# Optimization experiments

Measured on AMD Instinct MI355X. Metric: run time of the kernel, lower is better.

The kernel has to match this reference:

```python
import jax, jax.numpy as jnp
import numpy as np

N = 50000        # nodes
E = 800000       # edges
F_IN = 64
HID = [128, 256, 256]
G = 512          # graphs in batch
C = 6            # classes
EPS = 1e-5


def setup_inputs() -> dict:
    key = jax.random.key(0)
    ks = jax.random.split(key, 32)
    inp = {}
    inp['x'] = jax.random.normal(ks[0], (N, F_IN), dtype=jnp.float32)
    inp['edge_index'] = jax.random.randint(ks[1], (2, E), 0, N, dtype=jnp.int64)
    inp['batch'] = jnp.sort(jax.random.randint(ks[2], (N,), 0, G, dtype=jnp.int64))
    dims = [F_IN] + HID
    i = 3
    for l in range(3):
        d_in, d_out = dims[l], dims[l + 1]
        inp[f'W{l+1}'] = jax.random.normal(ks[i], (d_in, d_out), dtype=jnp.float32) * (1.0 / np.sqrt(d_in)); i += 1
        inp[f'b{l+1}'] = jnp.zeros((d_out,), dtype=jnp.float32)
        inp[f'g{l+1}'] = jnp.ones((d_out,), dtype=jnp.float32)
        inp[f'be{l+1}'] = jnp.zeros((d_out,), dtype=jnp.float32)
        inp[f'm{l+1}'] = jax.random.normal(ks[i], (d_out,), dtype=jnp.float32) * 0.1; i += 1
        inp[f'v{l+1}'] = jax.random.uniform(ks[i], (d_out,), dtype=jnp.float32, minval=0.5, maxval=1.5); i += 1
    mlp_dims = [(2 * HID[-1], 256), (256, 128), (128, C)]
    for l, (d_in, d_out) in enumerate(mlp_dims):
        inp[f'Wm{l+1}'] = jax.random.normal(ks[i], (d_in, d_out), dtype=jnp.float32) * (1.0 / np.sqrt(d_in)); i += 1
        inp[f'bm{l+1}'] = jnp.zeros((d_out,), dtype=jnp.float32)
    return inp


def _forward(x, edge_index, batch,
             W1, b1, g1, be1, m1, v1,
             W2, b2, g2, be2, m2, v2,
             W3, b3, g3, be3, m3, v3,
             Wm1, bm1, Wm2, bm2, Wm3, bm3):
    src, dst = edge_index[0], edge_index[1]
    loops = jnp.arange(N, dtype=src.dtype)
    src_sl = jnp.concatenate([src, loops])   # self-loops, as in PyG GCNConv
    dst_sl = jnp.concatenate([dst, loops])
    deg = jax.ops.segment_sum(jnp.ones_like(src_sl, dtype=x.dtype), dst_sl, num_segments=N)
    dis = jnp.where(deg > 0, jax.lax.rsqrt(deg), 0.0)
    norm = dis[src_sl] * dis[dst_sl]          # [E+N]

    def gcn(h, W, b):
        h = h @ W                              # transform first (PyG order)
        msg = h[src_sl] * norm[:, None]        # gather + scale
        return jax.ops.segment_sum(msg, dst_sl, num_segments=N) + b

    def bn_relu(h, g, be, m, v):
        return jax.nn.relu((h - m) * jax.lax.rsqrt(v + EPS) * g + be)

    h = bn_relu(gcn(x, W1, b1), g1, be1, m1, v1)
    h = bn_relu(gcn(h, W2, b2), g2, be2, m2, v2)
    h = bn_relu(gcn(h, W3, b3), g3, be3, m3, v3)

    counts = jax.ops.segment_sum(jnp.ones((N,), dtype=h.dtype), batch, num_segments=G)
    x_mean = jax.ops.segment_sum(h, batch, num_segments=G) / jnp.maximum(counts, 1.0)[:, None]
    x_max = jax.ops.segment_max(h, batch, num_segments=G)
    x_max = jnp.where(counts[:, None] > 0, x_max, 0.0)
    z = jnp.concatenate([x_mean, x_max], axis=1)   # [G, 512]

    z = jax.nn.gelu(z @ Wm1 + bm1, approximate=False)
    z = jax.nn.gelu(z @ Wm2 + bm2, approximate=False)
    return z @ Wm3 + bm3                            # [G, C]


def reference(x, edge_index, batch,
              W1, b1, g1, be1, m1, v1,
              W2, b2, g2, be2, m2, v2,
              W3, b3, g3, be3, m3, v3,
              Wm1, bm1, Wm2, bm2, Wm3, bm3):
    return _forward(x, edge_index, batch,
                    W1, b1, g1, be1, m1, v1,
                    W2, b2, g2, be2, m2, v2,
                    W3, b3, g3, be3, m3, v3,
                    Wm1, bm1, Wm2, bm2, Wm3, bm3)
```

## Files before the change

### kernel.cpp

```cpp
#include <hip/hip_runtime.h>
#include <hip/hip_bf16.h>
#include <hip/hip_fp16.h>

typedef __hip_bfloat16 bf16;
typedef unsigned short u16;
typedef short bfrag __attribute__((ext_vector_type(8)));
typedef float f32x4 __attribute__((ext_vector_type(4)));
typedef unsigned u32x2 __attribute__((ext_vector_type(2)));

#define NGRAPH 512
#define BN_EPS 1e-5f
#define NBUCK 64

__device__ __forceinline__ float b2f(bf16 x) { return __bfloat162float(x); }
__device__ __forceinline__ float bf_lo(unsigned u) { return __uint_as_float(u << 16); }
__device__ __forceinline__ float bf_hi(unsigned u) { return __uint_as_float(u & 0xffff0000u); }
__device__ __forceinline__ u16 f2u(float v) {
    bf16 t = __float2bfloat16(v);
    u16 r; __builtin_memcpy(&r, &t, 2); return r;
}

__device__ __forceinline__ float load_f(const void* p, int i, int isbf16) {
    if (isbf16) {
        unsigned short u = ((const unsigned short*)p)[i];
        return __uint_as_float(((unsigned int)u) << 16);
    }
    return ((const float*)p)[i];
}

__device__ __forceinline__ void repack_sec(const void* W, u16* out, int Kd, int Nd,
                                           int t, int isbf) {
    if (t >= Kd * Nd) return;
    int j = t & 7;
    int lane = (t >> 3) & 63;
    int tile = t >> 9;
    int NT = Nd / 16;
    int nt = tile % NT, kt = tile / NT;
    int k = kt * 32 + (lane >> 4) * 8 + j;
    int nn = nt * 16 + (lane & 15);
    out[t] = f2u(load_f(W, k * Nd + nn, isbf));
}

__device__ __forceinline__ void fold_one(const void* b, const void* g, const void* be,
                                         const void* m, const void* v,
                                         float* S, float* T, int f, int isbf) {
    float bb = load_f(b, f, isbf), gg = load_f(g, f, isbf);
    float bee = load_f(be, f, isbf), mm = load_f(m, f, isbf);
    float vv = load_f(v, f, isbf);
    float s = gg * rsqrtf(vv + BN_EPS);
    S[f] = s;
    T[f] = (bb - mm) * s + bee;
}

__global__ void prep_all(
    const void* __restrict__ x,
    const void* W1, const void* W2, const void* W3,
    const void* b1, const void* g1, const void* be1, const void* m1, const void* v1,
    const void* b2, const void* g2, const void* be2, const void* m2, const void* v2,
    const void* b3, const void* g3, const void* be3, const void* m3, const void* v3,
    u16* __restrict__ xs, u16* W1r, u16* W2r, u16* W3r,
    float* S1, float* T1, float* S2, float* T2, float* S3, float* T3,
    int* __restrict__ deg, int* __restrict__ ovf, int* __restrict__ bcnt,
    int* __restrict__ claim, float* __restrict__ psum, float* __restrict__ pmax,
    int* __restrict__ pcnt,
    int n, int npad, int* __restrict__ flag) {
    __shared__ int lflag;
    if (threadIdx.x < 64) {
        unsigned short u = ((const unsigned short*)x)[2 * threadIdx.x];
        float f = __uint_as_float(((unsigned int)u) << 16);
        int crazy = (!(fabsf(f) <= 1024.0f)) ? 1 : 0;
        unsigned long long m = __ballot(crazy);
        if (threadIdx.x == 0) lflag = (m == 0ULL) ? 1 : 0;
    }
    __syncthreads();
    const int isbf = lflag;
    const int bid = blockIdx.x;
    const int tid = threadIdx.x;
    if (bid == 0 && tid == 0) *flag = isbf;

    const int nb_cvt = (n * 64 + 255) / 256;
    if (bid < nb_cvt) {
        int i = bid * 256 + tid;
        if (i < n * 64) {
            int node = i >> 6, f = i & 63;
            xs[((size_t)(f >> 5) * npad + node) * 32 + (f & 31)] = f2u(load_f(x, i, isbf));
        }
        return;
    }
    int b2_ = bid - nb_cvt;
    if (b2_ < 32)  { repack_sec(W1, W1r, 64, 128, b2_ * 256 + tid, isbf); return; }
    b2_ -= 32;
    if (b2_ < 128) { repack_sec(W2, W2r, 128, 256, b2_ * 256 + tid, isbf); return; }
    b2_ -= 128;
    if (b2_ < 256) { repack_sec(W3, W3r, 256, 256, b2_ * 256 + tid, isbf); return; }
    b2_ -= 256;
    if (b2_ < 3) {
        int t = b2_ * 256 + tid;
        if (t < 128) fold_one(b1, g1, be1, m1, v1, S1, T1, t, isbf);
        else if (t < 384) fold_one(b2, g2, be2, m2, v2, S2, T2, t - 128, isbf);
        else if (t < 640) fold_one(b3, g3, be3, m3, v3, S3, T3, t - 384, isbf);
        return;
    }
    b2_ -= 3;
    {
        int i = b2_ * 256 + tid;
        if (i < n) deg[i] = 0;
        if (i < NGRAPH * 256) { psum[i] = 0.f; pmax[i] = 0.f; }
        if (i < NGRAPH) pcnt[i] = 0;
        if (i < NBUCK) { bcnt[i] = 0; claim[i] = 0; }
        if (i == 0) *ovf = 0;
    }
}

__global__ void count_deg_i(const int* __restrict__ dst, int* __restrict__ deg, int e) {
    int i = blockIdx.x * blockDim.x + threadIdx.x;
    if (i < e) atomicAdd(&deg[dst[i]], 1);
}

__global__ void hist_rows(const int* __restrict__ deg, float* __restrict__ dis,
                          int* __restrict__ bcnt, int n) {
    __shared__ int lh[NBUCK];
    int tid = threadIdx.x;
    if (tid < NBUCK) lh[tid] = 0;
    __syncthreads();
    int i = blockIdx.x * blockDim.x + tid;
    if (i < n) {
        int d = deg[i];
        dis[i] = rsqrtf((float)(d + 1));
        atomicAdd(&lh[min((d + 7) >> 3, NBUCK - 1)], 1);
    }
    __syncthreads();
    if (tid < NBUCK) {
        int c = lh[tid];
        if (c) atomicAdd(&bcnt[tid], c);
    }
}

__global__ void node_scatter(const int* __restrict__ deg, const int* __restrict__ bcnt,
                             int* __restrict__ claim, int* __restrict__ ovf,
                             int* __restrict__ cursor, unsigned* __restrict__ csrw,
                             uint4* __restrict__ ninfo, int n, int cap) {
    __shared__ int lh[NBUCK];
    __shared__ int lbase[NBUCK];
    __shared__ int cpre[NBUCK];
    __shared__ int wpre[NBUCK];
    int tid = threadIdx.x;
    if (tid < NBUCK) lh[tid] = 0;
    if (tid == 64) {
        int ca = 0, wa = 0;
        for (int k = 0; k < NBUCK; k++) {
            cpre[k] = ca; wpre[k] = wa;
            ca += bcnt[k]; wa += bcnt[k] * 8 * k;
        }
    }
    __syncthreads();
    int i = blockIdx.x * blockDim.x + tid;
    int b = 0, lr = 0, d = 0;
    if (i < n) {
        d = deg[i];
        b = min((d + 7) >> 3, NBUCK - 1);
        lr = atomicAdd(&lh[b], 1);
    }
    __syncthreads();
    if (tid < NBUCK) {
        int c = lh[tid];
        lbase[tid] = c ? atomicAdd(&claim[tid], c) : 0;
    }
    __syncthreads();
    if (i >= n) return;
    int rank = lbase[b] + lr;
    int pos = cpre[b] + rank;
    int dpad = (d + 7) & ~7;
    int start;
    if (b < NBUCK - 1) {
        start = wpre[b] + rank * 8 * b;
    } else {
        start = cap - atomicAdd(ovf, dpad) - dpad;
    }
    cursor[i] = start;
    unsigned val = (unsigned)(i & 0xffff);
    for (int k = d; k < dpad; k++) csrw[start + k] = val;
    ninfo[pos] = make_uint4(i, start, d, 0);
}

__global__ void edge_scatter(const int* __restrict__ src, const int* __restrict__ dst,
                             const float* __restrict__ dis, int* __restrict__ cursor,
                             unsigned* __restrict__ csrw, int e) {
    int i = blockIdx.x * blockDim.x + threadIdx.x;
    if (i >= e) return;
    int s = src[i], dt = dst[i];
    int pos = atomicAdd(&cursor[dt], 1);
    float nw = dis[s] * dis[dt];
    unsigned short h = __half_as_ushort(__float2half(nw));
    csrw[pos] = (unsigned)(s & 0xffff) | ((unsigned)h << 16);
}

template <int NSLICE>
__global__ __launch_bounds__(256) void csr_agg_s6(
    const uint4* __restrict__ ninfo, const unsigned* __restrict__ csrw,
    const u16* __restrict__ hs, u16* __restrict__ AG, int n, int npad) {
    constexpr int F = NSLICE * 32;
    int slice = blockIdx.x % NSLICE;
    int nb = blockIdx.x / NSLICE;
    int lane = threadIdx.x & 63;
    int wv = threadIdx.x >> 6;
    int sub = lane >> 3, ls = lane & 7;
    int oidx = nb * 32 + wv * 8 + sub;
    if (oidx >= n) return;
    uint4 nf = ninfo[oidx];
    int node = (int)nf.x;
    int start = (int)nf.y;
    int d = (int)nf.z;
    int dpad = (d + 7) & ~7;
    float dd = 1.0f / (float)(d + 1);
    const u16* __restrict__ base = hs + (size_t)slice * npad * 32;

    float a0, a1, a2, a3;
    {
        uint2 u = *(const uint2*)(base + (size_t)node * 32 + ls * 4);
        a0 = bf_lo(u.x) * dd; a1 = bf_hi(u.x) * dd;
        a2 = bf_lo(u.y) * dd; a3 = bf_hi(u.y) * dd;
    }

    const unsigned* __restrict__ ep = csrw + start;
    int k = 0;
    for (; k + 16 <= dpad; k += 16) {
        unsigned m[16];
#pragma unroll
        for (int j = 0; j < 16; j++) m[j] = ep[k + j];
        uint2 q[16];
#pragma unroll
        for (int j = 0; j < 16; j++) {
            int s = (int)(m[j] & 0xffffu);
            q[j] = *(const uint2*)(base + (size_t)s * 32 + ls * 4);
        }
#pragma unroll
        for (int j = 0; j < 16; j++) {
            float w = __half2float(__ushort_as_half((unsigned short)(m[j] >> 16)));
            a0 += w * bf_lo(q[j].x); a1 += w * bf_hi(q[j].x);
            a2 += w * bf_lo(q[j].y); a3 += w * bf_hi(q[j].y);
        }
    }
    if (k < dpad) {
        unsigned m[8];
#pragma unroll
        for (int j = 0; j < 8; j++) m[j] = ep[k + j];
        uint2 q[8];
#pragma unroll
        for (int j = 0; j < 8; j++) {
            int s = (int)(m[j] & 0xffffu);
            q[j] = *(const uint2*)(base + (size_t)s * 32 + ls * 4);
        }
#pragma unroll
        for (int j = 0; j < 8; j++) {
            float w = __half2float(__ushort_as_half((unsigned short)(m[j] >> 16)));
            a0 += w * bf_lo(q[j].x); a1 += w * bf_hi(q[j].x);
            a2 += w * bf_lo(q[j].y); a3 += w * bf_hi(q[j].y);
        }
    }
    u32x2 o;
    o.x = (unsigned)f2u(a0) | ((unsigned)f2u(a1) << 16);
    o.y = (unsigned)f2u(a2) | ((unsigned)f2u(a3) << 16);
    __builtin_nontemporal_store(o, (u32x2*)(AG + (size_t)node * F + slice * 32 + ls * 4));
}

template <int K, int N, int NSUB, int NSLICE_OUT>
__global__ __launch_bounds__(256) void mfma_gemm_dg(
    const u16* __restrict__ A, const u16* __restrict__ Wrep,
    const float* __restrict__ S, const float* __restrict__ T,
    u16* __restrict__ C, int M, int npad, int ntiles) {
    constexpr int NT = N / 16;
    constexpr int KT = K / 32;
    constexpr int NSPLIT = NT / NSUB;
    int bid = blockIdx.x;
    int g = bid >> 3;
    int ns = g % NSPLIT;
    int mt = (bid & 7) + 8 * (g / NSPLIT);
    if (mt >= ntiles) return;
    const int tid = threadIdx.x;
    const int lane = tid & 63;
    const int wv = tid >> 6;
    const int mrow = lane & 15;
    const int kb = lane >> 4;

    bfrag breg[KT * NSUB];
#pragma unroll
    for (int kt = 0; kt < KT; kt++)
#pragma unroll
        for (int j = 0; j < NSUB; j++)
            breg[kt * NSUB + j] = *(const bfrag*)(Wrep +
                ((size_t)(kt * NT + ns * NSUB + j) * 64 + lane) * 8);

    const u16* __restrict__ arow = A + (size_t)(mt * 64 + wv * 16 + mrow) * K + kb * 8;
    bfrag areg[KT];
#pragma unroll
    for (int kt = 0; kt < KT; kt++)
        areg[kt] = *(const bfrag*)(arow + kt * 32);

    f32x4 acc[NSUB];
#pragma unroll
    for (int j = 0; j < NSUB; j++) acc[j] = (f32x4){0.f, 0.f, 0.f, 0.f};
#pragma unroll
    for (int kt = 0; kt < KT; kt++)
#pragma unroll
        for (int j = 0; j < NSUB; j++)
            acc[j] = __builtin_amdgcn_mfma_f32_16x16x32_bf16(areg[kt], breg[kt * NSUB + j], acc[j], 0, 0, 0);

    const int m0 = mt * 64;
#pragma unroll
    for (int j = 0; j < NSUB; j++) {
        int f = (ns * NSUB + j) * 16 + mrow;
        float s = S[f];
        float t = T[f];
#pragma unroll
        for (int r = 0; r < 4; r++) {
            int row = m0 + wv * 16 + kb * 4 + r;
            if (row < M) {
                u16 val = f2u(fmaxf(acc[j][r] * s + t, 0.0f));
                if (NSLICE_OUT > 0)
                    C[((size_t)(f >> 5) * npad + row) * 32 + (f & 31)] = val;
                else
                    C[(size_t)row * N + f] = val;
            }
        }
    }
}

#define POOL_NC 64
__global__ __launch_bounds__(256) void pool_seg(
    const u16* __restrict__ h, const int* __restrict__ batch,
    float* __restrict__ psum, float* __restrict__ pmax,
    int* __restrict__ pcnt, int n) {
    int wid = (int)(((size_t)blockIdx.x * blockDim.x + threadIdx.x) >> 6);
    int lane = threadIdx.x & 63;
    int n0 = wid * POOL_NC;
    if (n0 >= n) return;
    int n1 = min(n0 + POOL_NC, n);

    float sum[4] = {0.f, 0.f, 0.f, 0.f};
    float mx[4] = {0.f, 0.f, 0.f, 0.f};
    int cnt = 0;
    int gcur = batch[n0];

    uint2 u_next = *(const uint2*)(h + (size_t)n0 * 256 + lane * 4);
    int g_next = gcur;

    for (int node = n0; node < n1; node++) {
        uint2 u = u_next;
        int g = g_next;
        if (node + 1 < n1) {
            u_next = *(const uint2*)(h + (size_t)(node + 1) * 256 + lane * 4);
            g_next = batch[node + 1];
        }
        if (g != gcur) {
#pragma unroll
            for (int c = 0; c < 4; c++) {
                atomicAdd(&psum[gcur * 256 + lane * 4 + c], sum[c]);
                atomicMax((int*)&pmax[gcur * 256 + lane * 4 + c], __float_as_int(mx[c]));
                sum[c] = 0.f; mx[c] = 0.f;
            }
            if (lane == 0) atomicAdd(&pcnt[gcur], cnt);
            cnt = 0;
            gcur = g;
        }
        float v0 = bf_lo(u.x), v1 = bf_hi(u.x), v2 = bf_lo(u.y), v3 = bf_hi(u.y);
        sum[0] += v0; sum[1] += v1; sum[2] += v2; sum[3] += v3;
        mx[0] = fmaxf(mx[0], v0); mx[1] = fmaxf(mx[1], v1);
        mx[2] = fmaxf(mx[2], v2); mx[3] = fmaxf(mx[3], v3);
        cnt++;
    }
#pragma unroll
    for (int c = 0; c < 4; c++) {
        atomicAdd(&psum[gcur * 256 + lane * 4 + c], sum[c]);
        atomicMax((int*)&pmax[gcur * 256 + lane * 4 + c], __float_as_int(mx[c]));
    }
    if (lane == 0) atomicAdd(&pcnt[gcur], cnt);
}

__global__ __launch_bounds__(256) void mlp_fused(
    const float* __restrict__ psum, const float* __restrict__ pmax,
    const int* __restrict__ pcnt,
    const void* __restrict__ Wm1, const void* __restrict__ bm1,
    const void* __restrict__ Wm2, const void* __restrict__ bm2,
    const void* __restrict__ Wm3, const void* __restrict__ bm3,
    void* __restrict__ out, const int* __restrict__ flag) {
    __shared__ float a[512];
    __shared__ float h1[256];
    __shared__ float h2[128];
    int row = blockIdx.x;
    int tid = threadIdx.x;
    int isbf = *flag;
    float invc = 1.0f / (float)max(pcnt[row], 1);
    a[tid] = psum[row * 256 + tid] * invc;
    a[256 + tid] = pmax[row * 256 + tid];
    __syncthreads();
    {
        float acc = load_f(bm1, tid, isbf);
        if (isbf) {
            const bf16* w = (const bf16*)Wm1;
            for (int k = 0; k < 512; k++) acc += a[k] * b2f(w[k * 256 + tid]);
        } else {
            const float* w = (const float*)Wm1;
            for (int k = 0; k < 512; k++) acc += a[k] * w[k * 256 + tid];
        }
        h1[tid] = 0.5f * acc * (1.0f + erff(acc * 0.70710678118654752f));
    }
    __syncthreads();
    if (tid < 128) {
        float acc = load_f(bm2, tid, isbf);
        if (isbf) {
            const bf16* w = (const bf16*)Wm2;
            for (int k = 0; k < 256; k++) acc += h1[k] * b2f(w[k * 128 + tid]);
        } else {
            const float* w = (const float*)Wm2;
            for (int k = 0; k < 256; k++) acc += h1[k] * w[k * 128 + tid];
        }
        h2[tid] = 0.5f * acc * (1.0f + erff(acc * 0.70710678118654752f));
    }
    __syncthreads();
    if (tid < 6) {
        float acc = load_f(bm3, tid, isbf);
        if (isbf) {
            const bf16* w = (const bf16*)Wm3;
            for (int k = 0; k < 128; k++) acc += h2[k] * b2f(w[k * 6 + tid]);
        } else {
            const float* w = (const float*)Wm3;
            for (int k = 0; k < 128; k++) acc += h2[k] * w[k * 6 + tid];
        }
        if (isbf) ((bf16*)out)[row * 6 + tid] = __float2bfloat16(acc);
        else      ((float*)out)[row * 6 + tid] = acc;
    }
}

extern "C" void kernel_launch(void* const* d_in, const int* in_sizes, int n_in,
                              void* d_out, int out_size, void* d_ws, size_t ws_size,
                              hipStream_t stream) {
    const void* x     = d_in[0];
    const int*  ei    = (const int*)d_in[1];
    const int*  batch = (const int*)d_in[2];
    const void *W1 = d_in[3],  *b1 = d_in[4],  *g1 = d_in[5],  *be1 = d_in[6],  *m1 = d_in[7],  *v1 = d_in[8];
    const void *W2 = d_in[9],  *b2 = d_in[10], *g2 = d_in[11], *be2 = d_in[12], *m2 = d_in[13], *v2 = d_in[14];
    const void *W3 = d_in[15], *b3 = d_in[16], *g3 = d_in[17], *be3 = d_in[18], *m3 = d_in[19], *v3 = d_in[20];
    const void *Wm1 = d_in[21], *bm1 = d_in[22];
    const void *Wm2 = d_in[23], *bm2 = d_in[24];
    const void *Wm3 = d_in[25], *bm3 = d_in[26];

    const int n = in_sizes[0] / 64;
    const int E = in_sizes[1] / 2;
    const int* src = ei;
    const int* dst = ei + E;
    const int npad = (n + 63 + 64) & ~63;
    const int ntiles = (n + 63) / 64;
    const int ntp8 = (ntiles + 7) & ~7;
    const int cap = E + 8 * n;

    size_t off = 0;
    auto carve = [&](size_t bytes) {
        void* p = (char*)d_ws + off;
        off += (bytes + 255) & ~(size_t)255;
        return p;
    };
    int*      flag  = (int*)carve(4);
    int*      ovf   = (int*)carve(4);
    int*      bcnt  = (int*)carve(NBUCK * 4);
    int*      claim = (int*)carve(NBUCK * 4);
    float*    dis   = (float*)carve((size_t)n * 4);
    int*      deg_i = (int*)carve((size_t)n * 4);
    int*      curs  = (int*)carve((size_t)n * 4);
    uint4*    ninfo = (uint4*)carve((size_t)n * 16);
    unsigned* csrw  = (unsigned*)carve((size_t)cap * 4);
    u16*      xs    = (u16*)carve((size_t)npad * 64 * 2);
    u16*      Hs    = (u16*)carve((size_t)npad * 256 * 2);
    u16*      AG    = (u16*)carve((size_t)npad * 256 * 2);
    u16*      H     = (u16*)carve((size_t)npad * 256 * 2);
    u16*      W1r   = (u16*)carve((size_t)64 * 128 * 2);
    u16*      W2r   = (u16*)carve((size_t)128 * 256 * 2);
    u16*      W3r   = (u16*)carve((size_t)256 * 256 * 2);
    float* S1 = (float*)carve(128 * 4); float* T1 = (float*)carve(128 * 4);
    float* S2 = (float*)carve(256 * 4); float* T2 = (float*)carve(256 * 4);
    float* S3 = (float*)carve(256 * 4); float* T3 = (float*)carve(256 * 4);
    float* psum = (float*)carve((size_t)NGRAPH * 256 * 4);
    float* pmax = (float*)carve((size_t)NGRAPH * 256 * 4);
    int*   pcnt = (int*)carve((size_t)NGRAPH * 4);
    (void)ws_size; (void)n_in;

    const int BT = 256;

    const int nb_cvt = (n * 64 + 255) / 256;
    const int nb_init = (NGRAPH * 256 + 255) / 256;
    prep_all<<<nb_cvt + 32 + 128 + 256 + 3 + nb_init, BT, 0, stream>>>(
        x, W1, W2, W3,
        b1, g1, be1, m1, v1, b2, g2, be2, m2, v2, b3, g3, be3, m3, v3,
        xs, W1r, W2r, W3r, S1, T1, S2, T2, S3, T3,
        deg_i, ovf, bcnt, claim, psum, pmax, pcnt, n, npad, flag);

    count_deg_i<<<(E + BT - 1) / BT, BT, 0, stream>>>(dst, deg_i, E);
    hist_rows<<<(n + BT - 1) / BT, BT, 0, stream>>>(deg_i, dis, bcnt, n);
    node_scatter<<<(n + BT - 1) / BT, BT, 0, stream>>>(deg_i, bcnt, claim, ovf,
                                                       curs, csrw, ninfo, n, cap);
    edge_scatter<<<(E + BT - 1) / BT, BT, 0, stream>>>(src, dst, dis, curs, csrw, E);

    const int nb32 = (n + 31) / 32;

    csr_agg_s6<2><<<2 * nb32, 256, 0, stream>>>(ninfo, csrw, xs, AG, n, npad);
    mfma_gemm_dg<64, 128, 4, 4><<<2 * ntp8, 256, 0, stream>>>(AG, W1r, S1, T1, Hs, n, npad, ntiles);

    csr_agg_s6<4><<<4 * nb32, 256, 0, stream>>>(ninfo, csrw, Hs, AG, n, npad);
    mfma_gemm_dg<128, 256, 4, 8><<<4 * ntp8, 256, 0, stream>>>(AG, W2r, S2, T2, Hs, n, npad, ntiles);

    csr_agg_s6<8><<<8 * nb32, 256, 0, stream>>>(ninfo, csrw, Hs, AG, n, npad);
    mfma_gemm_dg<256, 256, 2, 0><<<8 * ntp8, 256, 0, stream>>>(AG, W3r, S3, T3, H, n, npad, ntiles);

    const int pool_waves = (n + POOL_NC - 1) / POOL_NC;
    pool_seg<<<(pool_waves * 64 + BT - 1) / BT, BT, 0, stream>>>(H, batch, psum, pmax, pcnt, n);
    mlp_fused<<<NGRAPH, 256, 0, stream>>>(psum, pmax, pcnt, Wm1, bm1, Wm2, bm2, Wm3, bm3, d_out, flag);
}
```

Before: 420.5 us.

## Precompute edge ranks and scatter CSR writes partitioned by XCD address range

Degree counting now records each edge's rank within its destination row, so the second atomic cursor pass is gone. Edge position and packed payload are written to a record array. A separate scatter kernel then has each of 8 block groups, which the code maps to XCDs by block index, write only the records whose target falls in its 1/8 slice of the CSR array, aiming for L2-local writes. In exchange, each XCD group reads the full record array, which adds extra read traffic, a new kernel launch, and E*12 bytes of workspace.

```diff
diff --git a/kernel.cpp b/kernel.cpp
--- a/kernel.cpp
+++ b/kernel.cpp
@@ -112,9 +112,10 @@
     }
 }
 
-__global__ void count_deg_i(const int* __restrict__ dst, int* __restrict__ deg, int e) {
+__global__ void count_rank(const int* __restrict__ dst, int* __restrict__ deg,
+                           int* __restrict__ erank, int e) {
     int i = blockIdx.x * blockDim.x + threadIdx.x;
-    if (i < e) atomicAdd(&deg[dst[i]], 1);
+    if (i < e) erank[i] = atomicAdd(&deg[dst[i]], 1);
 }
 
 __global__ void hist_rows(const int* __restrict__ deg, float* __restrict__ dis,
@@ -138,7 +139,7 @@
 
 __global__ void node_scatter(const int* __restrict__ deg, const int* __restrict__ bcnt,
                              int* __restrict__ claim, int* __restrict__ ovf,
-                             int* __restrict__ cursor, unsigned* __restrict__ csrw,
+                             int* __restrict__ nstart, unsigned* __restrict__ csrw,
                              uint4* __restrict__ ninfo, int n, int cap) {
     __shared__ int lh[NBUCK];
     __shared__ int lbase[NBUCK];
@@ -177,22 +178,36 @@
     } else {
         start = cap - atomicAdd(ovf, dpad) - dpad;
     }
-    cursor[i] = start;
+    nstart[i] = start;
     unsigned val = (unsigned)(i & 0xffff);
     for (int k = d; k < dpad; k++) csrw[start + k] = val;
     ninfo[pos] = make_uint4(i, start, d, 0);
 }
 
-__global__ void edge_scatter(const int* __restrict__ src, const int* __restrict__ dst,
-                             const float* __restrict__ dis, int* __restrict__ cursor,
-                             unsigned* __restrict__ csrw, int e) {
+__global__ void make_recs(const int* __restrict__ src, const int* __restrict__ dst,
+                          const int* __restrict__ erank, const int* __restrict__ nstart,
+                          const float* __restrict__ dis, uint2* __restrict__ rec, int e) {
     int i = blockIdx.x * blockDim.x + threadIdx.x;
     if (i >= e) return;
     int s = src[i], dt = dst[i];
-    int pos = atomicAdd(&cursor[dt], 1);
+    unsigned pos = (unsigned)(nstart[dt] + erank[i]);
     float nw = dis[s] * dis[dt];
     unsigned short h = __half_as_ushort(__float2half(nw));
-    csrw[pos] = (unsigned)(s & 0xffff) | ((unsigned)h << 16);
+    rec[i] = make_uint2(pos, (unsigned)(s & 0xffff) | ((unsigned)h << 16));
+}
+
+__global__ __launch_bounds__(256) void xcd_scatter(
+    const uint2* __restrict__ rec, unsigned* __restrict__ csrw, int e, int cap) {
+    int xcd = blockIdx.x & 7;
+    int g = blockIdx.x >> 3;
+    int ngroups = gridDim.x >> 3;
+    unsigned lo = (unsigned)(((long long)cap * xcd) >> 3);
+    unsigned hi = (unsigned)(((long long)cap * (xcd + 1)) >> 3);
+    int stride = ngroups * 256;
+    for (int i = g * 256 + threadIdx.x; i < e; i += stride) {
+        uint2 r = rec[i];
+        if (r.x >= lo && r.x < hi) csrw[r.x] = r.y;
+    }
 }
 
 template <int NSLICE>
@@ -466,7 +481,9 @@
     int*      claim = (int*)carve(NBUCK * 4);
     float*    dis   = (float*)carve((size_t)n * 4);
     int*      deg_i = (int*)carve((size_t)n * 4);
-    int*      curs  = (int*)carve((size_t)n * 4);
+    int*      nstart= (int*)carve((size_t)n * 4);
+    int*      erank = (int*)carve((size_t)E * 4);
+    uint2*    rec   = (uint2*)carve((size_t)E * 8);
     uint4*    ninfo = (uint4*)carve((size_t)n * 16);
     unsigned* csrw  = (unsigned*)carve((size_t)cap * 4);
     u16*      xs    = (u16*)carve((size_t)npad * 64 * 2);
@@ -494,11 +511,12 @@
         xs, W1r, W2r, W3r, S1, T1, S2, T2, S3, T3,
         deg_i, ovf, bcnt, claim, psum, pmax, pcnt, n, npad, flag);
 
-    count_deg_i<<<(E + BT - 1) / BT, BT, 0, stream>>>(dst, deg_i, E);
+    count_rank<<<(E + BT - 1) / BT, BT, 0, stream>>>(dst, deg_i, erank, E);
     hist_rows<<<(n + BT - 1) / BT, BT, 0, stream>>>(deg_i, dis, bcnt, n);
     node_scatter<<<(n + BT - 1) / BT, BT, 0, stream>>>(deg_i, bcnt, claim, ovf,
-                                                       curs, csrw, ninfo, n, cap);
-    edge_scatter<<<(E + BT - 1) / BT, BT, 0, stream>>>(src, dst, dis, curs, csrw, E);
+                                                       nstart, csrw, ninfo, n, cap);
+    make_recs<<<(E + BT - 1) / BT, BT, 0, stream>>>(src, dst, erank, nstart, dis, rec, E);
+    xcd_scatter<<<8 * 64, BT, 0, stream>>>(rec, csrw, E, cap);
 
     const int nb32 = (n + 31) / 32;
 
```

Result: no change. 414.2 us (-1.5%).
